# Kernel tuning notes

Measured on AMD Instinct MI355X. Metric: run time of the kernel, lower is better.

The kernel has to match this reference:

```python
import jax, jax.numpy as jnp
import numpy as np

N_HEADS = 4


def setup_inputs() -> dict:
    key = jax.random.key(0)
    ks = jax.random.split(key, 8)
    T, B, V, F = 30, 64, 32, 128   # len_pred, batch, n_vehicles, feature_size
    L, LF, TH = 64, 64, 20         # n_lanes, lane_feature_size, len_hist
    vehicles = jax.random.normal(ks[0], (T, B, V, F), dtype=jnp.float32)
    lanes = jax.random.normal(ks[1], (B, V, L, LF), dtype=jnp.float32)
    mask_lanes = jax.random.randint(ks[2], (TH, B, V, L), 0, 2).astype(bool)
    # torch Linear weight layout [out, in]; conv 1x1 weights squeezed to [out, in]
    Wk = jax.random.normal(ks[3], (F, LF), dtype=jnp.float32) / np.sqrt(LF)
    Wv = jax.random.normal(ks[4], (F, LF), dtype=jnp.float32) / np.sqrt(LF)
    Wq = jax.random.normal(ks[5], (F, F), dtype=jnp.float32) / np.sqrt(F)
    Wc = jax.random.normal(ks[6], (F, F), dtype=jnp.float32) / np.sqrt(F)
    return {"vehicles": vehicles, "lanes": lanes, "mask_lanes": mask_lanes,
            "Wk": Wk, "Wv": Wv, "Wq": Wq, "Wc": Wc}


def reference(vehicles, lanes, mask_lanes, Wk, Wv, Wq, Wc):
    # vehicles: [T,B,V,F], lanes: [B,V,L,LF], mask_lanes: [TH,B,V,L] bool
    T, B, V, F = vehicles.shape
    L = lanes.shape[2]
    H = N_HEADS
    hd = F // H
    # Linear projections of lanes (torch Linear: y = x @ W.T)
    k = jnp.einsum('bvlf,gf->bvlg', lanes, Wk).reshape(B, V, L, H, hd)
    v = jnp.einsum('bvlf,gf->bvlg', lanes, Wv).reshape(B, V, L, H, hd)
    # 1x1 Conv2d on feature channels == per-position linear
    q = jnp.einsum('tbvf,gf->tbvg', vehicles, Wq).reshape(T, B, V, H, hd)
    # mask: any over history dim -> [B,V,L] (the second any in attention is a no-op
    # since the mask is repeated identically over T and heads)
    mask = jnp.any(mask_lanes, axis=0)  # [B,V,L]
    scores = jnp.einsum('tbvhd,bvlhd->tbvhl', q, k) / jnp.sqrt(jnp.float32(hd))
    scores = jnp.where(mask[None, :, :, None, :], scores, jnp.float32(-1e9))
    p = jax.nn.softmax(scores, axis=-1)  # [T,B,V,H,L]
    out = jnp.einsum('tbvhl,bvlhd->tbvhd', p, v).reshape(T, B, V, F)
    out = jnp.einsum('tbvf,gf->tbvg', out, Wc) + vehicles
    return out
```

## Files before the change

### kernel.cpp

```cpp
#include <hip/hip_runtime.h>
#include <hip/hip_bf16.h>

#define T_  30
#define B_  64
#define V_  32
#define F_  128
#define L_  64
#define LF_ 64
#define TH_ 20
#define H_  4
#define HD_ 32

typedef __attribute__((ext_vector_type(8))) short bf16x8;
typedef __attribute__((ext_vector_type(4))) short bf16x4;
typedef __attribute__((ext_vector_type(4))) float f32x4;
#define MFMA(a,b,c) __builtin_amdgcn_mfma_f32_16x16x32_bf16(a, b, c, 0, 0, 0)

__device__ __forceinline__ f32x4 mfma16(bf16x4 a, bf16x4 b, f32x4 c) {
#if defined(__HIP_DEVICE_COMPILE__)
    return __builtin_amdgcn_mfma_f32_16x16x16bf16_1k(a, b, c, 0, 0, 0);
#else
    (void)a; (void)b; return c;
#endif
}

__device__ __forceinline__ float bf1(unsigned short u) {
    unsigned int x = ((unsigned int)u) << 16; float f; __builtin_memcpy(&f, &x, 4); return f;
}
__device__ __forceinline__ unsigned int cvtpk(float a, float b) {
    __hip_bfloat162 h = __float22bfloat162_rn(make_float2(a, b));
    unsigned int r; __builtin_memcpy(&r, &h, 4); return r;
}
__device__ __forceinline__ void st4pk(unsigned short* p, float a, float b, float c, float d) {
    uint2 u = { cvtpk(a, b), cvtpk(c, d) };
    *(uint2*)p = u;
}
__device__ __forceinline__ int swz128(int r, int c) { return r * 128 + (c ^ ((r & 7) << 3)); }
__device__ __forceinline__ int swz64 (int r, int c) { return r * 64  + (c ^ ((r & 7) << 3)); }
__device__ __forceinline__ bf16x8 ldWfrag(const void* W, int off, bool isBf16) {
    if (isBf16) return *(const bf16x8*)((const unsigned short*)W + off);
    const float* p = (const float*)W + off;
    float4 a = *(const float4*)p;
    float4 b = *(const float4*)(p + 4);
    uint4 u = { cvtpk(a.x, a.y), cvtpk(a.z, a.w), cvtpk(b.x, b.y), cvtpk(b.z, b.w) };
    bf16x8 r; __builtin_memcpy(&r, &u, 16); return r;
}

__global__ __launch_bounds__(512, 8)
void lane_attn_kernel(const void* __restrict__ veh,
                      const void* __restrict__ lanes,
                      const void* __restrict__ maskp,
                      const void* __restrict__ Wk, const void* __restrict__ Wv,
                      const void* __restrict__ Wq, const void* __restrict__ Wc,
                      float* __restrict__ outp)
{
    const int bv    = blockIdx.x;
    const int tid   = threadIdx.x;
    const int w     = tid >> 6;
    const int h     = w >> 1;
    const int shalf = w & 1;
    const int lane  = tid & 63;
    const int quad  = lane >> 4;
    const int lm    = lane & 15;
    const int fbase = h * 32;
    const int fs    = fbase + shalf * 16;
    const int pfs   = fbase + (1 - shalf) * 16;

    __shared__ __align__(16) unsigned short sK   [8192];
    __shared__ __align__(16) unsigned short sReg1[8192];
    __shared__ __align__(16) unsigned short sReg2[4096];
    unsigned short* sLanes = sReg1;
    unsigned short* sVehB  = sReg1 + 4096;
    unsigned short* sVx    = sReg1;
    unsigned short* sQ     = sReg2;
    unsigned short* sO     = sReg2;

    const unsigned short* vh16 = (const unsigned short*)veh;
    const int field = (vh16[2 * lane] >> 7) & 0xFF;
    const bool isBf16 = __popcll(__ballot(field >= 100 && field <= 130)) >= 32;
    const unsigned char* mbp = (const unsigned char*)maskp;
    const bool maskByte = (__ballot(mbp[4 * lane + 1] != 0) != 0ULL);

    bool ok;
    {
        const int* mi = (const int*)maskp;
        int o = 0;
        #pragma unroll
        for (int th = 0; th < TH_; ++th) {
            const size_t e = (size_t)th * (B_ * V_ * L_) + (size_t)bv * L_ + lane;
            o |= maskByte ? (int)mbp[e] : mi[e];
        }
        ok = (o != 0);
    }
    const unsigned long long mok = __ballot(ok);

    if (isBf16) {
        {
            const int l = tid >> 3, g = tid & 7;
            uint4 x = *(const uint4*)((const unsigned short*)lanes + (size_t)bv * 4096 + tid * 8);
            *(uint4*)&sLanes[swz64(l, g * 8)] = x;
        }
        {
            const int t = tid >> 4, g = tid & 15;
            uint4 x = {0, 0, 0, 0};
            if (t < T_)
                x = *(const uint4*)((const unsigned short*)veh + ((size_t)t * (B_ * V_) + bv) * F_ + g * 8);
            *(uint4*)&sVehB[swz128(t, g * 8)] = x;
        }
    } else {
        const float4* lf4 = (const float4*)lanes;
        #pragma unroll
        for (int rr = 0; rr < 2; ++rr) {
            const int u = tid + rr * 512;
            const int l = u >> 4, c = (u & 15) * 4;
            float4 x = lf4[bv * 1024 + u];
            uint2 y = { cvtpk(x.x, x.y), cvtpk(x.z, x.w) };
            *(uint2*)&sLanes[swz64(l, c)] = y;
        }
        #pragma unroll
        for (int rr = 0; rr < 2; ++rr) {
            const int u = tid + rr * 512;
            const int t = u >> 5, c = (u & 31) * 4;
            uint2 y = {0, 0};
            if (t < T_) {
                float4 x = ((const float4*)veh)[((size_t)t * (B_ * V_) + bv) * 32 + (u & 31)];
                y.x = cvtpk(x.x, x.y); y.y = cvtpk(x.z, x.w);
            }
            *(uint2*)&sVehB[swz128(t, c)] = y;
        }
    }
    __syncthreads();

    {
        bf16x8 wbK[2];
        #pragma unroll
        for (int kt = 0; kt < 2; ++kt)
            wbK[kt] = ldWfrag(Wk, (fs + lm) * 64 + kt * 32 + quad * 8, isBf16);
        f32x4 accK[4];
        #pragma unroll
        for (int mt = 0; mt < 4; ++mt) accK[mt] = (f32x4)0.f;
        #pragma unroll
        for (int kt = 0; kt < 2; ++kt) {
            bf16x8 a[4];
            #pragma unroll
            for (int mt = 0; mt < 4; ++mt)
                a[mt] = *(const bf16x8*)&sLanes[swz64(mt * 16 + lm, kt * 32 + quad * 8)];
            #pragma unroll
            for (int mt = 0; mt < 4; ++mt) accK[mt] = MFMA(wbK[kt], a[mt], accK[mt]);
        }
        #pragma unroll
        for (int mt = 0; mt < 4; ++mt)
            st4pk(&sK[swz128(mt * 16 + lm, fs + quad * 4)],
                  accK[mt][0], accK[mt][1], accK[mt][2], accK[mt][3]);
    }

    bf16x4 vb[4];
    {
        bf16x8 wbV[2];
        #pragma unroll
        for (int kt = 0; kt < 2; ++kt)
            wbV[kt] = ldWfrag(Wv, (fs + lm) * 64 + kt * 32 + quad * 8, isBf16);
        f32x4 accV[4];
        #pragma unroll
        for (int mt = 0; mt < 4; ++mt) accV[mt] = (f32x4)0.f;
        #pragma unroll
        for (int kt = 0; kt < 2; ++kt) {
            bf16x8 a[4];
            #pragma unroll
            for (int mt = 0; mt < 4; ++mt)
                a[mt] = *(const bf16x8*)&sLanes[swz64(mt * 16 + lm, kt * 32 + quad * 8)];
            #pragma unroll
            for (int mt = 0; mt < 4; ++mt) accV[mt] = MFMA(a[mt], wbV[kt], accV[mt]);
        }
        #pragma unroll
        for (int mt = 0; mt < 4; ++mt) {
            uint2 y = { cvtpk(accV[mt][0], accV[mt][1]), cvtpk(accV[mt][2], accV[mt][3]) };
            __builtin_memcpy(&vb[mt], &y, 8);
        }
    }

    {
        bf16x8 wq[4];
        #pragma unroll
        for (int kt = 0; kt < 4; ++kt)
            wq[kt] = ldWfrag(Wq, (fs + lm) * 128 + kt * 32 + quad * 8, isBf16);
        f32x4 acc[2];
        acc[0] = (f32x4)0.f; acc[1] = (f32x4)0.f;
        #pragma unroll
        for (int kt = 0; kt < 4; ++kt) {
            bf16x8 b[2];
            #pragma unroll
            for (int nt = 0; nt < 2; ++nt)
                b[nt] = *(const bf16x8*)&sVehB[swz128(nt * 16 + lm, kt * 32 + quad * 8)];
            #pragma unroll
            for (int nt = 0; nt < 2; ++nt) acc[nt] = MFMA(wq[kt], b[nt], acc[nt]);
        }
        const float sc = 0.17677669529663687f;
        #pragma unroll
        for (int nt = 0; nt < 2; ++nt)
            st4pk(&sQ[swz128(nt * 16 + lm, fs + quad * 4)],
                  acc[nt][0] * sc, acc[nt][1] * sc, acc[nt][2] * sc, acc[nt][3] * sc);
    }
    __syncthreads();

    #pragma unroll
    for (int kt = 0; kt < 4; ++kt) {
        uint2 y; __builtin_memcpy(&y, &vb[kt], 8);
        *(uint2*)&sVx[w * 1024 + kt * 256 + lane * 4] = y;
    }

    bf16x4 pa[4];
    float inv;
    {
        bf16x8 a[4], b;
        #pragma unroll
        for (int mt = 0; mt < 4; ++mt)
            a[mt] = *(const bf16x8*)&sK[swz128(mt * 16 + lm, fbase + quad * 8)];
        b = *(const bf16x8*)&sQ[swz128(shalf * 16 + lm, fbase + quad * 8)];
        const int t = shalf * 16 + lm;
        const bool tok = (t < T_);
        const unsigned long long msh = (tok ? mok : 0ULL) >> (quad * 4);
        const unsigned int mlo = (unsigned int)msh, mhi = (unsigned int)(msh >> 32);
        float psum = 0.f;
        #pragma unroll
        for (int mt = 0; mt < 4; ++mt) {
            f32x4 acc = MFMA(a[mt], b, (f32x4)0.f);
            const unsigned int mw = (mt >= 2) ? mhi : mlo;
            const int bp = (mt * 16) & 31;
            float e0 = ((mw >> (bp + 0)) & 1u) ? __expf(acc[0]) : 0.f;
            float e1 = ((mw >> (bp + 1)) & 1u) ? __expf(acc[1]) : 0.f;
            float e2 = ((mw >> (bp + 2)) & 1u) ? __expf(acc[2]) : 0.f;
            float e3 = ((mw >> (bp + 3)) & 1u) ? __expf(acc[3]) : 0.f;
            psum += (e0 + e1) + (e2 + e3);
            uint2 y = { cvtpk(e0, e1), cvtpk(e2, e3) };
            __builtin_memcpy(&pa[mt], &y, 8);
        }
        psum += __shfl_xor(psum, 16, 64);
        psum += __shfl_xor(psum, 32, 64);
        inv = (psum > 0.f) ? 1.f / psum : 0.f;
    }
    __syncthreads();

    {
        f32x4 o0 = (f32x4)0.f, o1 = (f32x4)0.f;
        #pragma unroll
        for (int kt = 0; kt < 4; ++kt) {
            uint2 y = *(const uint2*)&sVx[(w ^ 1) * 1024 + kt * 256 + lane * 4];
            bf16x4 vx; __builtin_memcpy(&vx, &y, 8);
            o0 = mfma16(vb[kt], pa[kt], o0);
            o1 = mfma16(vx,     pa[kt], o1);
        }
        const int t = shalf * 16 + lm;
        st4pk(&sO[swz128(t, fs  + quad * 4)],
              o0[0] * inv, o0[1] * inv, o0[2] * inv, o0[3] * inv);
        st4pk(&sO[swz128(t, pfs + quad * 4)],
              o1[0] * inv, o1[1] * inv, o1[2] * inv, o1[3] * inv);
    }

    float4 res[2];
    #pragma unroll
    for (int nt = 0; nt < 2; ++nt) {
        const int t = nt * 16 + lm;
        res[nt] = make_float4(0.f, 0.f, 0.f, 0.f);
        if (t < T_) {
            const size_t off = ((size_t)t * (B_ * V_) + bv) * F_ + fs + quad * 4;
            if (isBf16) {
                ushort4 u = *(const ushort4*)((const unsigned short*)veh + off);
                res[nt] = make_float4(bf1(u.x), bf1(u.y), bf1(u.z), bf1(u.w));
            } else {
                res[nt] = *(const float4*)((const float*)veh + off);
            }
        }
    }
    __syncthreads();

    {
        bf16x8 wc[4];
        #pragma unroll
        for (int kt = 0; kt < 4; ++kt)
            wc[kt] = ldWfrag(Wc, (fs + lm) * 128 + kt * 32 + quad * 8, isBf16);
        f32x4 acc[2];
        acc[0] = (f32x4)0.f; acc[1] = (f32x4)0.f;
        #pragma unroll
        for (int kt = 0; kt < 4; ++kt) {
            bf16x8 b[2];
            #pragma unroll
            for (int nt = 0; nt < 2; ++nt)
                b[nt] = *(const bf16x8*)&sO[swz128(nt * 16 + lm, kt * 32 + quad * 8)];
            #pragma unroll
            for (int nt = 0; nt < 2; ++nt) acc[nt] = MFMA(wc[kt], b[nt], acc[nt]);
        }
        #pragma unroll
        for (int nt = 0; nt < 2; ++nt) {
            const int t = nt * 16 + lm;
            if (t < T_) {
                const size_t off = ((size_t)t * (B_ * V_) + bv) * F_ + fs + quad * 4;
                float4 o = make_float4(acc[nt][0] + res[nt].x, acc[nt][1] + res[nt].y,
                                       acc[nt][2] + res[nt].z, acc[nt][3] + res[nt].w);
                *(float4*)&outp[off] = o;
            }
        }
    }
}

extern "C" void kernel_launch(void* const* d_in, const int* in_sizes, int n_in,
                              void* d_out, int out_size, void* d_ws, size_t ws_size,
                              hipStream_t stream) {
    (void)in_sizes; (void)n_in; (void)out_size; (void)d_ws; (void)ws_size;
    lane_attn_kernel<<<dim3(B_ * V_), dim3(512), 0, stream>>>(
        d_in[0], d_in[1], d_in[2], d_in[3], d_in[4], d_in[5], d_in[6],
        (float*)d_out);
}
```

Measured before the change: 164.7 us.

## Process two (b,v) pairs per block with register prefetch of next inputs

Each block now handles two consecutive batch-vehicle pairs, so the grid is halved. The lane and vehicle tiles for the second pair are loaded into registers while the first pair is being computed, then written to shared memory at the start of the second iteration. The aim is to hide global load latency behind MFMA work and to spread per-block setup over two work items. In exchange it raises register pressure, which may lower occupancy, and it reduces the number of blocks available for the GPU to overlap latency across.

```diff
diff --git a/kernel.cpp b/kernel.cpp
--- a/kernel.cpp
+++ b/kernel.cpp
@@ -54,7 +54,7 @@
                       const void* __restrict__ Wq, const void* __restrict__ Wc,
                       float* __restrict__ outp)
 {
-    const int bv    = blockIdx.x;
+    const int bv0   = blockIdx.x * 2;
     const int tid   = threadIdx.x;
     const int w     = tid >> 6;
     const int h     = w >> 1;
@@ -81,223 +81,240 @@
     const unsigned char* mbp = (const unsigned char*)maskp;
     const bool maskByte = (__ballot(mbp[4 * lane + 1] != 0) != 0ULL);
 
-    bool ok;
-    {
-        const int* mi = (const int*)maskp;
-        int o = 0;
-        #pragma unroll
-        for (int th = 0; th < TH_; ++th) {
-            const size_t e = (size_t)th * (B_ * V_ * L_) + (size_t)bv * L_ + lane;
-            o |= maskByte ? (int)mbp[e] : mi[e];
-        }
-        ok = (o != 0);
-    }
-    const unsigned long long mok = __ballot(ok);
-
-    if (isBf16) {
-        {
-            const int l = tid >> 3, g = tid & 7;
-            uint4 x = *(const uint4*)((const unsigned short*)lanes + (size_t)bv * 4096 + tid * 8);
-            *(uint4*)&sLanes[swz64(l, g * 8)] = x;
-        }
-        {
+    float4 lpf0, lpf1, vpf0, vpf1;
+    uint4  lpb,  vpb;
+    auto issuePF = [&](int bvn) {
+        if (isBf16) {
+            lpb = *(const uint4*)((const unsigned short*)lanes + (size_t)bvn * 4096 + tid * 8);
             const int t = tid >> 4, g = tid & 15;
-            uint4 x = {0, 0, 0, 0};
+            uint4 z = {0, 0, 0, 0}; vpb = z;
             if (t < T_)
-                x = *(const uint4*)((const unsigned short*)veh + ((size_t)t * (B_ * V_) + bv) * F_ + g * 8);
-            *(uint4*)&sVehB[swz128(t, g * 8)] = x;
-        }
-    } else {
-        const float4* lf4 = (const float4*)lanes;
-        #pragma unroll
-        for (int rr = 0; rr < 2; ++rr) {
-            const int u = tid + rr * 512;
-            const int l = u >> 4, c = (u & 15) * 4;
-            float4 x = lf4[bv * 1024 + u];
-            uint2 y = { cvtpk(x.x, x.y), cvtpk(x.z, x.w) };
-            *(uint2*)&sLanes[swz64(l, c)] = y;
-        }
-        #pragma unroll
-        for (int rr = 0; rr < 2; ++rr) {
-            const int u = tid + rr * 512;
-            const int t = u >> 5, c = (u & 31) * 4;
-            uint2 y = {0, 0};
-            if (t < T_) {
-                float4 x = ((const float4*)veh)[((size_t)t * (B_ * V_) + bv) * 32 + (u & 31)];
-                y.x = cvtpk(x.x, x.y); y.y = cvtpk(x.z, x.w);
-            }
-            *(uint2*)&sVehB[swz128(t, c)] = y;
-        }
-    }
-    __syncthreads();
-
-    {
-        bf16x8 wbK[2];
-        #pragma unroll
-        for (int kt = 0; kt < 2; ++kt)
-            wbK[kt] = ldWfrag(Wk, (fs + lm) * 64 + kt * 32 + quad * 8, isBf16);
-        f32x4 accK[4];
-        #pragma unroll
-        for (int mt = 0; mt < 4; ++mt) accK[mt] = (f32x4)0.f;
-        #pragma unroll
-        for (int kt = 0; kt < 2; ++kt) {
-            bf16x8 a[4];
+                vpb = *(const uint4*)((const unsigned short*)veh + ((size_t)t * (B_ * V_) + bv0) * F_
+                                      + (size_t)(bvn - bv0) * F_ + g * 8);
+        } else {
+            const float4* lf4 = (const float4*)lanes;
+            lpf0 = lf4[bvn * 1024 + tid];
+            lpf1 = lf4[bvn * 1024 + tid + 512];
+            vpf0 = make_float4(0.f, 0.f, 0.f, 0.f);
+            vpf1 = vpf0;
+            {   const int u = tid;        const int t = u >> 5;
+                if (t < T_) vpf0 = ((const float4*)veh)[((size_t)t * (B_ * V_) + bvn) * 32 + (u & 31)]; }
+            {   const int u = tid + 512;  const int t = u >> 5;
+                if (t < T_) vpf1 = ((const float4*)veh)[((size_t)t * (B_ * V_) + bvn) * 32 + (u & 31)]; }
+        }
+    };
+    auto stageWrite = [&]() {
+        if (isBf16) {
+            *(uint4*)&sLanes[swz64(tid >> 3, (tid & 7) * 8)] = lpb;
+            *(uint4*)&sVehB[swz128(tid >> 4, (tid & 15) * 8)] = vpb;
+        } else {
+            {   const int u = tid;       const int l = u >> 4, c = (u & 15) * 4;
+                uint2 y = { cvtpk(lpf0.x, lpf0.y), cvtpk(lpf0.z, lpf0.w) };
+                *(uint2*)&sLanes[swz64(l, c)] = y; }
+            {   const int u = tid + 512; const int l = u >> 4, c = (u & 15) * 4;
+                uint2 y = { cvtpk(lpf1.x, lpf1.y), cvtpk(lpf1.z, lpf1.w) };
+                *(uint2*)&sLanes[swz64(l, c)] = y; }
+            {   const int u = tid;       const int t = u >> 5, c = (u & 31) * 4;
+                uint2 y = { cvtpk(vpf0.x, vpf0.y), cvtpk(vpf0.z, vpf0.w) };
+                *(uint2*)&sVehB[swz128(t, c)] = y; }
+            {   const int u = tid + 512; const int t = u >> 5, c = (u & 31) * 4;
+                uint2 y = { cvtpk(vpf1.x, vpf1.y), cvtpk(vpf1.z, vpf1.w) };
+                *(uint2*)&sVehB[swz128(t, c)] = y; }
+        }
+    };
+
+    issuePF(bv0);
+
+    #pragma unroll
+    for (int it = 0; it < 2; ++it) {
+        const int bv = bv0 + it;
+
+        bool ok;
+        {
+            const int* mi = (const int*)maskp;
+            int o = 0;
+            #pragma unroll
+            for (int th = 0; th < TH_; ++th) {
+                const size_t e = (size_t)th * (B_ * V_ * L_) + (size_t)bv * L_ + lane;
+                o |= maskByte ? (int)mbp[e] : mi[e];
+            }
+            ok = (o != 0);
+        }
+        const unsigned long long mok = __ballot(ok);
+
+        stageWrite();
+        __syncthreads();
+
+        if (it == 0) issuePF(bv0 + 1);
+
+        {
+            bf16x8 wbK[2];
+            #pragma unroll
+            for (int kt = 0; kt < 2; ++kt)
+                wbK[kt] = ldWfrag(Wk, (fs + lm) * 64 + kt * 32 + quad * 8, isBf16);
+            f32x4 accK[4];
+            #pragma unroll
+            for (int mt = 0; mt < 4; ++mt) accK[mt] = (f32x4)0.f;
+            #pragma unroll
+            for (int kt = 0; kt < 2; ++kt) {
+                bf16x8 a[4];
+                #pragma unroll
+                for (int mt = 0; mt < 4; ++mt)
+                    a[mt] = *(const bf16x8*)&sLanes[swz64(mt * 16 + lm, kt * 32 + quad * 8)];
+                #pragma unroll
+                for (int mt = 0; mt < 4; ++mt) accK[mt] = MFMA(wbK[kt], a[mt], accK[mt]);
+            }
             #pragma unroll
             for (int mt = 0; mt < 4; ++mt)
-                a[mt] = *(const bf16x8*)&sLanes[swz64(mt * 16 + lm, kt * 32 + quad * 8)];
-            #pragma unroll
-            for (int mt = 0; mt < 4; ++mt) accK[mt] = MFMA(wbK[kt], a[mt], accK[mt]);
-        }
-        #pragma unroll
-        for (int mt = 0; mt < 4; ++mt)
-            st4pk(&sK[swz128(mt * 16 + lm, fs + quad * 4)],
-                  accK[mt][0], accK[mt][1], accK[mt][2], accK[mt][3]);
-    }
-
-    bf16x4 vb[4];
-    {
-        bf16x8 wbV[2];
-        #pragma unroll
-        for (int kt = 0; kt < 2; ++kt)
-            wbV[kt] = ldWfrag(Wv, (fs + lm) * 64 + kt * 32 + quad * 8, isBf16);
-        f32x4 accV[4];
-        #pragma unroll
-        for (int mt = 0; mt < 4; ++mt) accV[mt] = (f32x4)0.f;
-        #pragma unroll
-        for (int kt = 0; kt < 2; ++kt) {
-            bf16x8 a[4];
-            #pragma unroll
-            for (int mt = 0; mt < 4; ++mt)
-                a[mt] = *(const bf16x8*)&sLanes[swz64(mt * 16 + lm, kt * 32 + quad * 8)];
-            #pragma unroll
-            for (int mt = 0; mt < 4; ++mt) accV[mt] = MFMA(a[mt], wbV[kt], accV[mt]);
-        }
-        #pragma unroll
-        for (int mt = 0; mt < 4; ++mt) {
-            uint2 y = { cvtpk(accV[mt][0], accV[mt][1]), cvtpk(accV[mt][2], accV[mt][3]) };
-            __builtin_memcpy(&vb[mt], &y, 8);
-        }
-    }
-
-    {
-        bf16x8 wq[4];
-        #pragma unroll
-        for (int kt = 0; kt < 4; ++kt)
-            wq[kt] = ldWfrag(Wq, (fs + lm) * 128 + kt * 32 + quad * 8, isBf16);
-        f32x4 acc[2];
-        acc[0] = (f32x4)0.f; acc[1] = (f32x4)0.f;
+                st4pk(&sK[swz128(mt * 16 + lm, fs + quad * 4)],
+                      accK[mt][0], accK[mt][1], accK[mt][2], accK[mt][3]);
+        }
+
+        bf16x4 vb[4];
+        {
+            bf16x8 wbV[2];
+            #pragma unroll
+            for (int kt = 0; kt < 2; ++kt)
+                wbV[kt] = ldWfrag(Wv, (fs + lm) * 64 + kt * 32 + quad * 8, isBf16);
+            f32x4 accV[4];
+            #pragma unroll
+            for (int mt = 0; mt < 4; ++mt) accV[mt] = (f32x4)0.f;
+            #pragma unroll
+            for (int kt = 0; kt < 2; ++kt) {
+                bf16x8 a[4];
+                #pragma unroll
+                for (int mt = 0; mt < 4; ++mt)
+                    a[mt] = *(const bf16x8*)&sLanes[swz64(mt * 16 + lm, kt * 32 + quad * 8)];
+                #pragma unroll
+                for (int mt = 0; mt < 4; ++mt) accV[mt] = MFMA(a[mt], wbV[kt], accV[mt]);
+            }
+            #pragma unroll
+            for (int mt = 0; mt < 4; ++mt) {
+                uint2 y = { cvtpk(accV[mt][0], accV[mt][1]), cvtpk(accV[mt][2], accV[mt][3]) };
+                __builtin_memcpy(&vb[mt], &y, 8);
+            }
+        }
+
+        {
+            bf16x8 wq[4];
+            #pragma unroll
+            for (int kt = 0; kt < 4; ++kt)
+                wq[kt] = ldWfrag(Wq, (fs + lm) * 128 + kt * 32 + quad * 8, isBf16);
+            f32x4 acc[2];
+            acc[0] = (f32x4)0.f; acc[1] = (f32x4)0.f;
+            #pragma unroll
+            for (int kt = 0; kt < 4; ++kt) {
+                bf16x8 b[2];
+                #pragma unroll
+                for (int nt = 0; nt < 2; ++nt)
+                    b[nt] = *(const bf16x8*)&sVehB[swz128(nt * 16 + lm, kt * 32 + quad * 8)];
+                #pragma unroll
+                for (int nt = 0; nt < 2; ++nt) acc[nt] = MFMA(wq[kt], b[nt], acc[nt]);
+            }
+            const float sc = 0.17677669529663687f;
+            #pragma unroll
+            for (int nt = 0; nt < 2; ++nt)
+                st4pk(&sQ[swz128(nt * 16 + lm, fs + quad * 4)],
+                      acc[nt][0] * sc, acc[nt][1] * sc, acc[nt][2] * sc, acc[nt][3] * sc);
+        }
+        __syncthreads();
+
         #pragma unroll
         for (int kt = 0; kt < 4; ++kt) {
-            bf16x8 b[2];
-            #pragma unroll
-            for (int nt = 0; nt < 2; ++nt)
-                b[nt] = *(const bf16x8*)&sVehB[swz128(nt * 16 + lm, kt * 32 + quad * 8)];
-            #pragma unroll
-            for (int nt = 0; nt < 2; ++nt) acc[nt] = MFMA(wq[kt], b[nt], acc[nt]);
-        }
-        const float sc = 0.17677669529663687f;
-        #pragma unroll
-        for (int nt = 0; nt < 2; ++nt)
-            st4pk(&sQ[swz128(nt * 16 + lm, fs + quad * 4)],
-                  acc[nt][0] * sc, acc[nt][1] * sc, acc[nt][2] * sc, acc[nt][3] * sc);
-    }
-    __syncthreads();
-
-    #pragma unroll
-    for (int kt = 0; kt < 4; ++kt) {
-        uint2 y; __builtin_memcpy(&y, &vb[kt], 8);
-        *(uint2*)&sVx[w * 1024 + kt * 256 + lane * 4] = y;
-    }
-
-    bf16x4 pa[4];
-    float inv;
-    {
-        bf16x8 a[4], b;
-        #pragma unroll
-        for (int mt = 0; mt < 4; ++mt)
-            a[mt] = *(const bf16x8*)&sK[swz128(mt * 16 + lm, fbase + quad * 8)];
-        b = *(const bf16x8*)&sQ[swz128(shalf * 16 + lm, fbase + quad * 8)];
-        const int t = shalf * 16 + lm;
-        const bool tok = (t < T_);
-        const unsigned long long msh = (tok ? mok : 0ULL) >> (quad * 4);
-        const unsigned int mlo = (unsigned int)msh, mhi = (unsigned int)(msh >> 32);
-        float psum = 0.f;
-        #pragma unroll
-        for (int mt = 0; mt < 4; ++mt) {
-            f32x4 acc = MFMA(a[mt], b, (f32x4)0.f);
-            const unsigned int mw = (mt >= 2) ? mhi : mlo;
-            const int bp = (mt * 16) & 31;
-            float e0 = ((mw >> (bp + 0)) & 1u) ? __expf(acc[0]) : 0.f;
-            float e1 = ((mw >> (bp + 1)) & 1u) ? __expf(acc[1]) : 0.f;
-            float e2 = ((mw >> (bp + 2)) & 1u) ? __expf(acc[2]) : 0.f;
-            float e3 = ((mw >> (bp + 3)) & 1u) ? __expf(acc[3]) : 0.f;
-            psum += (e0 + e1) + (e2 + e3);
-            uint2 y = { cvtpk(e0, e1), cvtpk(e2, e3) };
-            __builtin_memcpy(&pa[mt], &y, 8);
-        }
-        psum += __shfl_xor(psum, 16, 64);
-        psum += __shfl_xor(psum, 32, 64);
-        inv = (psum > 0.f) ? 1.f / psum : 0.f;
-    }
-    __syncthreads();
-
-    {
-        f32x4 o0 = (f32x4)0.f, o1 = (f32x4)0.f;
-        #pragma unroll
-        for (int kt = 0; kt < 4; ++kt) {
-            uint2 y = *(const uint2*)&sVx[(w ^ 1) * 1024 + kt * 256 + lane * 4];
-            bf16x4 vx; __builtin_memcpy(&vx, &y, 8);
-            o0 = mfma16(vb[kt], pa[kt], o0);
-            o1 = mfma16(vx,     pa[kt], o1);
-        }
-        const int t = shalf * 16 + lm;
-        st4pk(&sO[swz128(t, fs  + quad * 4)],
-              o0[0] * inv, o0[1] * inv, o0[2] * inv, o0[3] * inv);
-        st4pk(&sO[swz128(t, pfs + quad * 4)],
-              o1[0] * inv, o1[1] * inv, o1[2] * inv, o1[3] * inv);
-    }
-
-    float4 res[2];
-    #pragma unroll
-    for (int nt = 0; nt < 2; ++nt) {
-        const int t = nt * 16 + lm;
-        res[nt] = make_float4(0.f, 0.f, 0.f, 0.f);
-        if (t < T_) {
-            const size_t off = ((size_t)t * (B_ * V_) + bv) * F_ + fs + quad * 4;
-            if (isBf16) {
-                ushort4 u = *(const ushort4*)((const unsigned short*)veh + off);
-                res[nt] = make_float4(bf1(u.x), bf1(u.y), bf1(u.z), bf1(u.w));
-            } else {
-                res[nt] = *(const float4*)((const float*)veh + off);
-            }
-        }
-    }
-    __syncthreads();
-
-    {
-        bf16x8 wc[4];
-        #pragma unroll
-        for (int kt = 0; kt < 4; ++kt)
-            wc[kt] = ldWfrag(Wc, (fs + lm) * 128 + kt * 32 + quad * 8, isBf16);
-        f32x4 acc[2];
-        acc[0] = (f32x4)0.f; acc[1] = (f32x4)0.f;
-        #pragma unroll
-        for (int kt = 0; kt < 4; ++kt) {
-            bf16x8 b[2];
-            #pragma unroll
-            for (int nt = 0; nt < 2; ++nt)
-                b[nt] = *(const bf16x8*)&sO[swz128(nt * 16 + lm, kt * 32 + quad * 8)];
-            #pragma unroll
-            for (int nt = 0; nt < 2; ++nt) acc[nt] = MFMA(wc[kt], b[nt], acc[nt]);
-        }
+            uint2 y; __builtin_memcpy(&y, &vb[kt], 8);
+            *(uint2*)&sVx[w * 1024 + kt * 256 + lane * 4] = y;
+        }
+
+        bf16x4 pa[4];
+        float inv;
+        {
+            bf16x8 a[4], b;
+            #pragma unroll
+            for (int mt = 0; mt < 4; ++mt)
+                a[mt] = *(const bf16x8*)&sK[swz128(mt * 16 + lm, fbase + quad * 8)];
+            b = *(const bf16x8*)&sQ[swz128(shalf * 16 + lm, fbase + quad * 8)];
+            const int t = shalf * 16 + lm;
+            const bool tok = (t < T_);
+            const unsigned long long msh = (tok ? mok : 0ULL) >> (quad * 4);
+            const unsigned int mlo = (unsigned int)msh, mhi = (unsigned int)(msh >> 32);
+            float psum = 0.f;
+            #pragma unroll
+            for (int mt = 0; mt < 4; ++mt) {
+                f32x4 acc = MFMA(a[mt], b, (f32x4)0.f);
+                const unsigned int mw = (mt >= 2) ? mhi : mlo;
+                const int bp = (mt * 16) & 31;
+                float e0 = ((mw >> (bp + 0)) & 1u) ? __expf(acc[0]) : 0.f;
+                float e1 = ((mw >> (bp + 1)) & 1u) ? __expf(acc[1]) : 0.f;
+                float e2 = ((mw >> (bp + 2)) & 1u) ? __expf(acc[2]) : 0.f;
+                float e3 = ((mw >> (bp + 3)) & 1u) ? __expf(acc[3]) : 0.f;
+                psum += (e0 + e1) + (e2 + e3);
+                uint2 y = { cvtpk(e0, e1), cvtpk(e2, e3) };
+                __builtin_memcpy(&pa[mt], &y, 8);
+            }
+            psum += __shfl_xor(psum, 16, 64);
+            psum += __shfl_xor(psum, 32, 64);
+            inv = (psum > 0.f) ? 1.f / psum : 0.f;
+        }
+        __syncthreads();
+
+        {
+            f32x4 o0 = (f32x4)0.f, o1 = (f32x4)0.f;
+            #pragma unroll
+            for (int kt = 0; kt < 4; ++kt) {
+                uint2 y = *(const uint2*)&sVx[(w ^ 1) * 1024 + kt * 256 + lane * 4];
+                bf16x4 vx; __builtin_memcpy(&vx, &y, 8);
+                o0 = mfma16(vb[kt], pa[kt], o0);
+                o1 = mfma16(vx,     pa[kt], o1);
+            }
+            const int t = shalf * 16 + lm;
+            st4pk(&sO[swz128(t, fs  + quad * 4)],
+                  o0[0] * inv, o0[1] * inv, o0[2] * inv, o0[3] * inv);
+            st4pk(&sO[swz128(t, pfs + quad * 4)],
+                  o1[0] * inv, o1[1] * inv, o1[2] * inv, o1[3] * inv);
+        }
+
+        float4 res[2];
         #pragma unroll
         for (int nt = 0; nt < 2; ++nt) {
             const int t = nt * 16 + lm;
+            res[nt] = make_float4(0.f, 0.f, 0.f, 0.f);
             if (t < T_) {
                 const size_t off = ((size_t)t * (B_ * V_) + bv) * F_ + fs + quad * 4;
-                float4 o = make_float4(acc[nt][0] + res[nt].x, acc[nt][1] + res[nt].y,
-                                       acc[nt][2] + res[nt].z, acc[nt][3] + res[nt].w);
-                *(float4*)&outp[off] = o;
+                if (isBf16) {
+                    ushort4 u = *(const ushort4*)((const unsigned short*)veh + off);
+                    res[nt] = make_float4(bf1(u.x), bf1(u.y), bf1(u.z), bf1(u.w));
+                } else {
+                    res[nt] = *(const float4*)((const float*)veh + off);
+                }
+            }
+        }
+        __syncthreads();
+
+        {
+            bf16x8 wc[4];
+            #pragma unroll
+            for (int kt = 0; kt < 4; ++kt)
+                wc[kt] = ldWfrag(Wc, (fs + lm) * 128 + kt * 32 + quad * 8, isBf16);
+            f32x4 acc[2];
+            acc[0] = (f32x4)0.f; acc[1] = (f32x4)0.f;
+            #pragma unroll
+            for (int kt = 0; kt < 4; ++kt) {
+                bf16x8 b[2];
+                #pragma unroll
+                for (int nt = 0; nt < 2; ++nt)
+                    b[nt] = *(const bf16x8*)&sO[swz128(nt * 16 + lm, kt * 32 + quad * 8)];
+                #pragma unroll
+                for (int nt = 0; nt < 2; ++nt) acc[nt] = MFMA(wc[kt], b[nt], acc[nt]);
+            }
+            #pragma unroll
+            for (int nt = 0; nt < 2; ++nt) {
+                const int t = nt * 16 + lm;
+                if (t < T_) {
+                    const size_t off = ((size_t)t * (B_ * V_) + bv) * F_ + fs + quad * 4;
+                    float4 o = make_float4(acc[nt][0] + res[nt].x, acc[nt][1] + res[nt].y,
+                                           acc[nt][2] + res[nt].z, acc[nt][3] + res[nt].w);
+                    *(float4*)&outp[off] = o;
+                }
             }
         }
     }
@@ -307,7 +324,7 @@
                               void* d_out, int out_size, void* d_ws, size_t ws_size,
                               hipStream_t stream) {
     (void)in_sizes; (void)n_in; (void)out_size; (void)d_ws; (void)ws_size;
-    lane_attn_kernel<<<dim3(B_ * V_), dim3(512), 0, stream>>>(
+    lane_attn_kernel<<<dim3(B_ * V_ / 2), dim3(512), 0, stream>>>(
         d_in[0], d_in[1], d_in[2], d_in[3], d_in[4], d_in[5], d_in[6],
         (float*)d_out);
 }
```

Result: slower. 204.9 us (+24.4%).

## Process four vehicle pairs per block with async double-buffered staging

Applied to the files above, without the earlier changes.

Each block now loops over four (batch, vehicle) pairs, loading Wk/Wv weight fragments once and reusing them. For bf16 inputs it adds global_load_lds double buffering to prefetch the next pair's lanes and vehicles while computing the current one. V is computed for both head halves per wave, which removes the LDS exchange and a barrier. The cost is fewer blocks, a lower occupancy bound and more LDS per block. For float32 inputs the staging stays synchronous.

```diff
diff --git a/kernel.cpp b/kernel.cpp
--- a/kernel.cpp
+++ b/kernel.cpp
@@ -10,6 +10,7 @@
 #define TH_ 20
 #define H_  4
 #define HD_ 32
+#define G_  4
 
 typedef __attribute__((ext_vector_type(8))) short bf16x8;
 typedef __attribute__((ext_vector_type(4))) short bf16x4;
@@ -23,6 +24,19 @@
     (void)a; (void)b; return c;
 #endif
 }
+
+__device__ __forceinline__ void gld16(const void* g, unsigned short* l) {
+#if defined(__HIP_DEVICE_COMPILE__)
+    __builtin_amdgcn_global_load_lds(
+        (const __attribute__((address_space(1))) unsigned int*)g,
+        (__attribute__((address_space(3))) unsigned int*)l, 16, 0, 0);
+#else
+    (void)g; (void)l;
+#endif
+}
+
+#define BAR_VM()  asm volatile("s_waitcnt vmcnt(0) lgkmcnt(0)\n\ts_barrier" ::: "memory")
+#define BAR_LDS() asm volatile("s_waitcnt lgkmcnt(0)\n\ts_barrier" ::: "memory")
 
 __device__ __forceinline__ float bf1(unsigned short u) {
     unsigned int x = ((unsigned int)u) << 16; float f; __builtin_memcpy(&f, &x, 4); return f;
@@ -46,7 +60,7 @@
     bf16x8 r; __builtin_memcpy(&r, &u, 16); return r;
 }
 
-__global__ __launch_bounds__(512, 8)
+__global__ __launch_bounds__(512, 4)
 void lane_attn_kernel(const void* __restrict__ veh,
                       const void* __restrict__ lanes,
                       const void* __restrict__ maskp,
@@ -54,7 +68,7 @@
                       const void* __restrict__ Wq, const void* __restrict__ Wc,
                       float* __restrict__ outp)
 {
-    const int bv    = blockIdx.x;
+    const int bv0   = blockIdx.x * G_;
     const int tid   = threadIdx.x;
     const int w     = tid >> 6;
     const int h     = w >> 1;
@@ -66,14 +80,10 @@
     const int fs    = fbase + shalf * 16;
     const int pfs   = fbase + (1 - shalf) * 16;
 
-    __shared__ __align__(16) unsigned short sK   [8192];
-    __shared__ __align__(16) unsigned short sReg1[8192];
-    __shared__ __align__(16) unsigned short sReg2[4096];
-    unsigned short* sLanes = sReg1;
-    unsigned short* sVehB  = sReg1 + 4096;
-    unsigned short* sVx    = sReg1;
-    unsigned short* sQ     = sReg2;
-    unsigned short* sO     = sReg2;
+    __shared__ __align__(16) unsigned short sK  [8192];
+    __shared__ __align__(16) unsigned short sQ  [4096];
+    __shared__ __align__(16) unsigned short sO  [4096];
+    __shared__ __align__(16) unsigned short sStg[16384];
 
     const unsigned short* vh16 = (const unsigned short*)veh;
     const int field = (vh16[2 * lane] >> 7) & 0xFF;
@@ -81,41 +91,53 @@
     const unsigned char* mbp = (const unsigned char*)maskp;
     const bool maskByte = (__ballot(mbp[4 * lane + 1] != 0) != 0ULL);
 
-    bool ok;
-    {
+    if (tid >= 480) {
+        uint4 z = {0, 0, 0, 0};
+        *(uint4*)&sStg[tid * 8 + 4096] = z;
+        *(uint4*)&sStg[8192 + tid * 8 + 4096] = z;
+    }
+
+    unsigned long long mokA[G_];
+    #pragma unroll
+    for (int g = 0; g < G_; ++g) {
         const int* mi = (const int*)maskp;
         int o = 0;
         #pragma unroll
         for (int th = 0; th < TH_; ++th) {
-            const size_t e = (size_t)th * (B_ * V_ * L_) + (size_t)bv * L_ + lane;
+            const size_t e = (size_t)th * (B_ * V_ * L_) + (size_t)(bv0 + g) * L_ + lane;
             o |= maskByte ? (int)mbp[e] : mi[e];
         }
-        ok = (o != 0);
+        mokA[g] = __ballot(o != 0);
     }
-    const unsigned long long mok = __ballot(ok);
-
-    if (isBf16) {
-        {
-            const int l = tid >> 3, g = tid & 7;
-            uint4 x = *(const uint4*)((const unsigned short*)lanes + (size_t)bv * 4096 + tid * 8);
-            *(uint4*)&sLanes[swz64(l, g * 8)] = x;
-        }
-        {
-            const int t = tid >> 4, g = tid & 15;
-            uint4 x = {0, 0, 0, 0};
-            if (t < T_)
-                x = *(const uint4*)((const unsigned short*)veh + ((size_t)t * (B_ * V_) + bv) * F_ + g * 8);
-            *(uint4*)&sVehB[swz128(t, g * 8)] = x;
-        }
-    } else {
+
+    bf16x8 wbK[2], wbVo[2], wbVp[2];
+    #pragma unroll
+    for (int kt = 0; kt < 2; ++kt) {
+        wbK[kt]  = ldWfrag(Wk, (fs  + lm) * 64 + kt * 32 + quad * 8, isBf16);
+        wbVo[kt] = ldWfrag(Wv, (fs  + lm) * 64 + kt * 32 + quad * 8, isBf16);
+        wbVp[kt] = ldWfrag(Wv, (pfs + lm) * 64 + kt * 32 + quad * 8, isBf16);
+    }
+
+    const int sl_l = tid >> 3, sl_g = (tid & 7)  ^ (sl_l & 7);
+    const int sv_t = tid >> 4, sv_g = (tid & 15) ^ (sv_t & 7);
+    const unsigned short* lanesU = (const unsigned short*)lanes;
+    const unsigned short* vehU   = (const unsigned short*)veh;
+    auto stageIssue = [&](int buf, int bvn) {
+        gld16(lanesU + (size_t)bvn * 4096 + sl_l * 64 + sl_g * 8,
+              &sStg[buf * 8192 + w * 512]);
+        if (sv_t < T_)
+            gld16(vehU + ((size_t)sv_t * (B_ * V_) + bvn) * 128 + sv_g * 8,
+                  &sStg[buf * 8192 + 4096 + w * 512]);
+    };
+    auto stageF32 = [&](int buf, int bvn) {
         const float4* lf4 = (const float4*)lanes;
         #pragma unroll
         for (int rr = 0; rr < 2; ++rr) {
             const int u = tid + rr * 512;
             const int l = u >> 4, c = (u & 15) * 4;
-            float4 x = lf4[bv * 1024 + u];
+            float4 x = lf4[bvn * 1024 + u];
             uint2 y = { cvtpk(x.x, x.y), cvtpk(x.z, x.w) };
-            *(uint2*)&sLanes[swz64(l, c)] = y;
+            *(uint2*)&sStg[buf * 8192 + swz64(l, c)] = y;
         }
         #pragma unroll
         for (int rr = 0; rr < 2; ++rr) {
@@ -123,181 +145,190 @@
             const int t = u >> 5, c = (u & 31) * 4;
             uint2 y = {0, 0};
             if (t < T_) {
-                float4 x = ((const float4*)veh)[((size_t)t * (B_ * V_) + bv) * 32 + (u & 31)];
+                float4 x = ((const float4*)veh)[((size_t)t * (B_ * V_) + bvn) * 32 + (u & 31)];
                 y.x = cvtpk(x.x, x.y); y.y = cvtpk(x.z, x.w);
             }
-            *(uint2*)&sVehB[swz128(t, c)] = y;
-        }
-    }
-    __syncthreads();
-
-    {
-        bf16x8 wbK[2];
-        #pragma unroll
-        for (int kt = 0; kt < 2; ++kt)
-            wbK[kt] = ldWfrag(Wk, (fs + lm) * 64 + kt * 32 + quad * 8, isBf16);
-        f32x4 accK[4];
-        #pragma unroll
-        for (int mt = 0; mt < 4; ++mt) accK[mt] = (f32x4)0.f;
-        #pragma unroll
-        for (int kt = 0; kt < 2; ++kt) {
-            bf16x8 a[4];
+            *(uint2*)&sStg[buf * 8192 + 4096 + swz128(t, c)] = y;
+        }
+    };
+
+    if (isBf16) stageIssue(0, bv0);
+
+    #pragma unroll
+    for (int it = 0; it < G_; ++it) {
+        const int cur = it & 1;
+        const int bv  = bv0 + it;
+        const unsigned long long mok = mokA[it];
+        const unsigned short* sLanes = &sStg[cur * 8192];
+        const unsigned short* sVehB  = &sStg[cur * 8192 + 4096];
+
+        if (isBf16) {
+            BAR_VM();
+            if (it < G_ - 1) stageIssue(cur ^ 1, bv + 1);
+        } else {
+            stageF32(cur, bv);
+            BAR_VM();
+        }
+
+        {
+            f32x4 accK[4];
+            #pragma unroll
+            for (int mt = 0; mt < 4; ++mt) accK[mt] = (f32x4)0.f;
+            #pragma unroll
+            for (int kt = 0; kt < 2; ++kt) {
+                bf16x8 a[4];
+                #pragma unroll
+                for (int mt = 0; mt < 4; ++mt)
+                    a[mt] = *(const bf16x8*)&sLanes[swz64(mt * 16 + lm, kt * 32 + quad * 8)];
+                #pragma unroll
+                for (int mt = 0; mt < 4; ++mt) accK[mt] = MFMA(wbK[kt], a[mt], accK[mt]);
+            }
             #pragma unroll
             for (int mt = 0; mt < 4; ++mt)
-                a[mt] = *(const bf16x8*)&sLanes[swz64(mt * 16 + lm, kt * 32 + quad * 8)];
-            #pragma unroll
-            for (int mt = 0; mt < 4; ++mt) accK[mt] = MFMA(wbK[kt], a[mt], accK[mt]);
-        }
-        #pragma unroll
-        for (int mt = 0; mt < 4; ++mt)
-            st4pk(&sK[swz128(mt * 16 + lm, fs + quad * 4)],
-                  accK[mt][0], accK[mt][1], accK[mt][2], accK[mt][3]);
-    }
-
-    bf16x4 vb[4];
-    {
-        bf16x8 wbV[2];
-        #pragma unroll
-        for (int kt = 0; kt < 2; ++kt)
-            wbV[kt] = ldWfrag(Wv, (fs + lm) * 64 + kt * 32 + quad * 8, isBf16);
-        f32x4 accV[4];
-        #pragma unroll
-        for (int mt = 0; mt < 4; ++mt) accV[mt] = (f32x4)0.f;
-        #pragma unroll
-        for (int kt = 0; kt < 2; ++kt) {
-            bf16x8 a[4];
+                st4pk(&sK[swz128(mt * 16 + lm, fs + quad * 4)],
+                      accK[mt][0], accK[mt][1], accK[mt][2], accK[mt][3]);
+        }
+
+        bf16x4 vb[4], vx[4];
+        {
+            f32x4 aco[4], acp[4];
+            #pragma unroll
+            for (int mt = 0; mt < 4; ++mt) { aco[mt] = (f32x4)0.f; acp[mt] = (f32x4)0.f; }
+            #pragma unroll
+            for (int kt = 0; kt < 2; ++kt) {
+                bf16x8 a[4];
+                #pragma unroll
+                for (int mt = 0; mt < 4; ++mt)
+                    a[mt] = *(const bf16x8*)&sLanes[swz64(mt * 16 + lm, kt * 32 + quad * 8)];
+                #pragma unroll
+                for (int mt = 0; mt < 4; ++mt) {
+                    aco[mt] = MFMA(a[mt], wbVo[kt], aco[mt]);
+                    acp[mt] = MFMA(a[mt], wbVp[kt], acp[mt]);
+                }
+            }
+            #pragma unroll
+            for (int mt = 0; mt < 4; ++mt) {
+                uint2 yo = { cvtpk(aco[mt][0], aco[mt][1]), cvtpk(aco[mt][2], aco[mt][3]) };
+                uint2 yp = { cvtpk(acp[mt][0], acp[mt][1]), cvtpk(acp[mt][2], acp[mt][3]) };
+                __builtin_memcpy(&vb[mt], &yo, 8);
+                __builtin_memcpy(&vx[mt], &yp, 8);
+            }
+        }
+
+        {
+            bf16x8 wq[4];
+            #pragma unroll
+            for (int kt = 0; kt < 4; ++kt)
+                wq[kt] = ldWfrag(Wq, (fs + lm) * 128 + kt * 32 + quad * 8, isBf16);
+            f32x4 acc[2];
+            acc[0] = (f32x4)0.f; acc[1] = (f32x4)0.f;
+            #pragma unroll
+            for (int kt = 0; kt < 4; ++kt) {
+                bf16x8 b[2];
+                #pragma unroll
+                for (int nt = 0; nt < 2; ++nt)
+                    b[nt] = *(const bf16x8*)&sVehB[swz128(nt * 16 + lm, kt * 32 + quad * 8)];
+                #pragma unroll
+                for (int nt = 0; nt < 2; ++nt) acc[nt] = MFMA(wq[kt], b[nt], acc[nt]);
+            }
+            const float sc = 0.17677669529663687f;
+            #pragma unroll
+            for (int nt = 0; nt < 2; ++nt)
+                st4pk(&sQ[swz128(nt * 16 + lm, fs + quad * 4)],
+                      acc[nt][0] * sc, acc[nt][1] * sc, acc[nt][2] * sc, acc[nt][3] * sc);
+        }
+        BAR_LDS();
+
+        bf16x4 pa[4];
+        float inv;
+        {
+            bf16x8 a[4], b;
             #pragma unroll
             for (int mt = 0; mt < 4; ++mt)
-                a[mt] = *(const bf16x8*)&sLanes[swz64(mt * 16 + lm, kt * 32 + quad * 8)];
-            #pragma unroll
-            for (int mt = 0; mt < 4; ++mt) accV[mt] = MFMA(a[mt], wbV[kt], accV[mt]);
-        }
-        #pragma unroll
-        for (int mt = 0; mt < 4; ++mt) {
-            uint2 y = { cvtpk(accV[mt][0], accV[mt][1]), cvtpk(accV[mt][2], accV[mt][3]) };
-            __builtin_memcpy(&vb[mt], &y, 8);
-        }
-    }
-
-    {
-        bf16x8 wq[4];
-        #pragma unroll
-        for (int kt = 0; kt < 4; ++kt)
-            wq[kt] = ldWfrag(Wq, (fs + lm) * 128 + kt * 32 + quad * 8, isBf16);
-        f32x4 acc[2];
-        acc[0] = (f32x4)0.f; acc[1] = (f32x4)0.f;
-        #pragma unroll
-        for (int kt = 0; kt < 4; ++kt) {
-            bf16x8 b[2];
-            #pragma unroll
-            for (int nt = 0; nt < 2; ++nt)
-                b[nt] = *(const bf16x8*)&sVehB[swz128(nt * 16 + lm, kt * 32 + quad * 8)];
-            #pragma unroll
-            for (int nt = 0; nt < 2; ++nt) acc[nt] = MFMA(wq[kt], b[nt], acc[nt]);
-        }
-        const float sc = 0.17677669529663687f;
-        #pragma unroll
-        for (int nt = 0; nt < 2; ++nt)
-            st4pk(&sQ[swz128(nt * 16 + lm, fs + quad * 4)],
-                  acc[nt][0] * sc, acc[nt][1] * sc, acc[nt][2] * sc, acc[nt][3] * sc);
-    }
-    __syncthreads();
-
-    #pragma unroll
-    for (int kt = 0; kt < 4; ++kt) {
-        uint2 y; __builtin_memcpy(&y, &vb[kt], 8);
-        *(uint2*)&sVx[w * 1024 + kt * 256 + lane * 4] = y;
-    }
-
-    bf16x4 pa[4];
-    float inv;
-    {
-        bf16x8 a[4], b;
-        #pragma unroll
-        for (int mt = 0; mt < 4; ++mt)
-            a[mt] = *(const bf16x8*)&sK[swz128(mt * 16 + lm, fbase + quad * 8)];
-        b = *(const bf16x8*)&sQ[swz128(shalf * 16 + lm, fbase + quad * 8)];
-        const int t = shalf * 16 + lm;
-        const bool tok = (t < T_);
-        const unsigned long long msh = (tok ? mok : 0ULL) >> (quad * 4);
-        const unsigned int mlo = (unsigned int)msh, mhi = (unsigned int)(msh >> 32);
-        float psum = 0.f;
-        #pragma unroll
-        for (int mt = 0; mt < 4; ++mt) {
-            f32x4 acc = MFMA(a[mt], b, (f32x4)0.f);
-            const unsigned int mw = (mt >= 2) ? mhi : mlo;
-            const int bp = (mt * 16) & 31;
-            float e0 = ((mw >> (bp + 0)) & 1u) ? __expf(acc[0]) : 0.f;
-            float e1 = ((mw >> (bp + 1)) & 1u) ? __expf(acc[1]) : 0.f;
-            float e2 = ((mw >> (bp + 2)) & 1u) ? __expf(acc[2]) : 0.f;
-            float e3 = ((mw >> (bp + 3)) & 1u) ? __expf(acc[3]) : 0.f;
-            psum += (e0 + e1) + (e2 + e3);
-            uint2 y = { cvtpk(e0, e1), cvtpk(e2, e3) };
-            __builtin_memcpy(&pa[mt], &y, 8);
-        }
-        psum += __shfl_xor(psum, 16, 64);
-        psum += __shfl_xor(psum, 32, 64);
-        inv = (psum > 0.f) ? 1.f / psum : 0.f;
-    }
-    __syncthreads();
-
-    {
-        f32x4 o0 = (f32x4)0.f, o1 = (f32x4)0.f;
-        #pragma unroll
-        for (int kt = 0; kt < 4; ++kt) {
-            uint2 y = *(const uint2*)&sVx[(w ^ 1) * 1024 + kt * 256 + lane * 4];
-            bf16x4 vx; __builtin_memcpy(&vx, &y, 8);
-            o0 = mfma16(vb[kt], pa[kt], o0);
-            o1 = mfma16(vx,     pa[kt], o1);
-        }
-        const int t = shalf * 16 + lm;
-        st4pk(&sO[swz128(t, fs  + quad * 4)],
-              o0[0] * inv, o0[1] * inv, o0[2] * inv, o0[3] * inv);
-        st4pk(&sO[swz128(t, pfs + quad * 4)],
-              o1[0] * inv, o1[1] * inv, o1[2] * inv, o1[3] * inv);
-    }
-
-    float4 res[2];
-    #pragma unroll
-    for (int nt = 0; nt < 2; ++nt) {
-        const int t = nt * 16 + lm;
-        res[nt] = make_float4(0.f, 0.f, 0.f, 0.f);
-        if (t < T_) {
-            const size_t off = ((size_t)t * (B_ * V_) + bv) * F_ + fs + quad * 4;
-            if (isBf16) {
-                ushort4 u = *(const ushort4*)((const unsigned short*)veh + off);
-                res[nt] = make_float4(bf1(u.x), bf1(u.y), bf1(u.z), bf1(u.w));
-            } else {
-                res[nt] = *(const float4*)((const float*)veh + off);
-            }
-        }
-    }
-    __syncthreads();
-
-    {
-        bf16x8 wc[4];
-        #pragma unroll
-        for (int kt = 0; kt < 4; ++kt)
-            wc[kt] = ldWfrag(Wc, (fs + lm) * 128 + kt * 32 + quad * 8, isBf16);
-        f32x4 acc[2];
-        acc[0] = (f32x4)0.f; acc[1] = (f32x4)0.f;
-        #pragma unroll
-        for (int kt = 0; kt < 4; ++kt) {
-            bf16x8 b[2];
-            #pragma unroll
-            for (int nt = 0; nt < 2; ++nt)
-                b[nt] = *(const bf16x8*)&sO[swz128(nt * 16 + lm, kt * 32 + quad * 8)];
-            #pragma unroll
-            for (int nt = 0; nt < 2; ++nt) acc[nt] = MFMA(wc[kt], b[nt], acc[nt]);
-        }
+                a[mt] = *(const bf16x8*)&sK[swz128(mt * 16 + lm, fbase + quad * 8)];
+            b = *(const bf16x8*)&sQ[swz128(shalf * 16 + lm, fbase + quad * 8)];
+            const int t = shalf * 16 + lm;
+            const bool tok = (t < T_);
+            const unsigned long long msh = (tok ? mok : 0ULL) >> (quad * 4);
+            const unsigned int mlo = (unsigned int)msh, mhi = (unsigned int)(msh >> 32);
+            float psum = 0.f;
+            #pragma unroll
+            for (int mt = 0; mt < 4; ++mt) {
+                f32x4 acc = MFMA(a[mt], b, (f32x4)0.f);
+                const unsigned int mw = (mt >= 2) ? mhi : mlo;
+                const int bp = (mt * 16) & 31;
+                float e0 = ((mw >> (bp + 0)) & 1u) ? __expf(acc[0]) : 0.f;
+                float e1 = ((mw >> (bp + 1)) & 1u) ? __expf(acc[1]) : 0.f;
+                float e2 = ((mw >> (bp + 2)) & 1u) ? __expf(acc[2]) : 0.f;
+                float e3 = ((mw >> (bp + 3)) & 1u) ? __expf(acc[3]) : 0.f;
+                psum += (e0 + e1) + (e2 + e3);
+                uint2 y = { cvtpk(e0, e1), cvtpk(e2, e3) };
+                __builtin_memcpy(&pa[mt], &y, 8);
+            }
+            psum += __shfl_xor(psum, 16, 64);
+            psum += __shfl_xor(psum, 32, 64);
+            inv = (psum > 0.f) ? 1.f / psum : 0.f;
+        }
+
+        {
+            f32x4 o0 = (f32x4)0.f, o1 = (f32x4)0.f;
+            #pragma unroll
+            for (int kt = 0; kt < 4; ++kt) {
+                o0 = mfma16(vb[kt], pa[kt], o0);
+                o1 = mfma16(vx[kt], pa[kt], o1);
+            }
+            const int t = shalf * 16 + lm;
+            st4pk(&sO[swz128(t, fs  + quad * 4)],
+                  o0[0] * inv, o0[1] * inv, o0[2] * inv, o0[3] * inv);
+            st4pk(&sO[swz128(t, pfs + quad * 4)],
+                  o1[0] * inv, o1[1] * inv, o1[2] * inv, o1[3] * inv);
+        }
+
+        float4 res[2];
         #pragma unroll
         for (int nt = 0; nt < 2; ++nt) {
             const int t = nt * 16 + lm;
-            if (t < T_) {
-                const size_t off = ((size_t)t * (B_ * V_) + bv) * F_ + fs + quad * 4;
-                float4 o = make_float4(acc[nt][0] + res[nt].x, acc[nt][1] + res[nt].y,
-                                       acc[nt][2] + res[nt].z, acc[nt][3] + res[nt].w);
-                *(float4*)&outp[off] = o;
+            if (isBf16) {
+                uint2 y = *(const uint2*)&sVehB[swz128(t, fs + quad * 4)];
+                res[nt] = make_float4(bf1((unsigned short)(y.x & 0xFFFF)),
+                                      bf1((unsigned short)(y.x >> 16)),
+                                      bf1((unsigned short)(y.y & 0xFFFF)),
+                                      bf1((unsigned short)(y.y >> 16)));
+            } else {
+                res[nt] = make_float4(0.f, 0.f, 0.f, 0.f);
+                if (t < T_) {
+                    const size_t off = ((size_t)t * (B_ * V_) + bv) * F_ + fs + quad * 4;
+                    res[nt] = *(const float4*)((const float*)veh + off);
+                }
+            }
+        }
+        BAR_LDS();
+
+        {
+            bf16x8 wc[4];
+            #pragma unroll
+            for (int kt = 0; kt < 4; ++kt)
+                wc[kt] = ldWfrag(Wc, (fs + lm) * 128 + kt * 32 + quad * 8, isBf16);
+            f32x4 acc[2];
+            acc[0] = (f32x4)0.f; acc[1] = (f32x4)0.f;
+            #pragma unroll
+            for (int kt = 0; kt < 4; ++kt) {
+                bf16x8 b[2];
+                #pragma unroll
+                for (int nt = 0; nt < 2; ++nt)
+                    b[nt] = *(const bf16x8*)&sO[swz128(nt * 16 + lm, kt * 32 + quad * 8)];
+                #pragma unroll
+                for (int nt = 0; nt < 2; ++nt) acc[nt] = MFMA(wc[kt], b[nt], acc[nt]);
+            }
+            #pragma unroll
+            for (int nt = 0; nt < 2; ++nt) {
+                const int t = nt * 16 + lm;
+                if (t < T_) {
+                    const size_t off = ((size_t)t * (B_ * V_) + bv) * F_ + fs + quad * 4;
+                    float4 o = make_float4(acc[nt][0] + res[nt].x, acc[nt][1] + res[nt].y,
+                                           acc[nt][2] + res[nt].z, acc[nt][3] + res[nt].w);
+                    *(float4*)&outp[off] = o;
+                }
             }
         }
     }
@@ -307,7 +338,7 @@
                               void* d_out, int out_size, void* d_ws, size_t ws_size,
                               hipStream_t stream) {
     (void)in_sizes; (void)n_in; (void)out_size; (void)d_ws; (void)ws_size;
-    lane_attn_kernel<<<dim3(B_ * V_), dim3(512), 0, stream>>>(
+    lane_attn_kernel<<<dim3(B_ * V_ / G_), dim3(512), 0, stream>>>(
         d_in[0], d_in[1], d_in[2], d_in[3], d_in[4], d_in[5], d_in[6],
         (float*)d_out);
 }
```

Measured after the change: 167.2 us. About the same (+1.5%).
